# Performance work log

Measured on AMD Instinct MI355X. Metric: run time of the kernel, lower is better.

Reference implementation:

```python
import jax, jax.numpy as jnp
import numpy as np
import math

D_MODEL = 1024
N_HEADS = 16
HEAD_DIM = D_MODEL // N_HEADS
RANK = 128
SCALE = 1.0 / math.sqrt(HEAD_DIM)


def lowrank(x, u, v, b):
    # y = (x @ u) @ v + b : d_model -> rank -> d_model
    return jnp.einsum('bsd,dr,re->bse', x, u, v) + b


def setup_inputs() -> dict:
    key = jax.random.key(0)
    ks = jax.random.split(key, 16)
    B, S = 2, 2048
    inp = {
        'q': jax.random.normal(ks[0], (B, S, D_MODEL), jnp.float32),
        'k': jax.random.normal(ks[1], (B, S, D_MODEL), jnp.float32),
        'v': jax.random.normal(ks[2], (B, S, D_MODEL), jnp.float32),
        'mask': jnp.ones((B, S), jnp.int32),
    }
    i = 3
    for name in ('q', 'k', 'v', 'out'):
        inp[f'{name}_u'] = jax.random.normal(ks[i], (D_MODEL, RANK), jnp.float32) * 0.02
        inp[f'{name}_v'] = jax.random.normal(ks[i + 1], (RANK, D_MODEL), jnp.float32) * 0.02
        inp[f'{name}_b'] = jnp.zeros((D_MODEL,), jnp.float32)
        i += 2
    return inp


def reference(q, k, v, mask, q_u, q_v, q_b, k_u, k_v, k_b, v_u, v_v, v_b, out_u, out_v, out_b):
    B, S, _ = q.shape
    qh = lowrank(q, q_u, q_v, q_b).reshape(B, S, N_HEADS, HEAD_DIM)
    kh = lowrank(k, k_u, k_v, k_b).reshape(B, S, N_HEADS, HEAD_DIM)
    vh = lowrank(v, v_u, v_v, v_b).reshape(B, S, N_HEADS, HEAD_DIM)
    # scores: [B, H, Sq, Sk]
    scores = jnp.einsum('bqhd,bkhd->bhqk', qh, kh) * SCALE
    scores = jnp.where(mask[:, None, None, :] == 0, -1e9, scores)
    attn = jax.nn.softmax(scores, axis=-1)
    ctx = jnp.einsum('bhqk,bkhd->bqhd', attn, vh).reshape(B, S, D_MODEL)
    return lowrank(ctx, out_u, out_v, out_b)
```

## Files before the change

### kernel.cpp

```cpp
#include <hip/hip_runtime.h>
#include <hip/hip_bf16.h>
#include <stdint.h>

#define DEVI __device__ __forceinline__

typedef __attribute__((ext_vector_type(8))) __bf16 bf16x8;
typedef __attribute__((ext_vector_type(4))) float f32x4;
typedef __attribute__((ext_vector_type(4))) unsigned short us4;

DEVI unsigned short f2bf(float x) {
  union { __bf16 b; unsigned short s; } u;
  u.b = (__bf16)x;
  return u.s;
}

DEVI f32x4 mfma16(bf16x8 a, bf16x8 b, f32x4 c) {
  return __builtin_amdgcn_mfma_f32_16x16x32_bf16(a, b, c, 0, 0, 0);
}

DEVI f32x4 vmax4(f32x4 a, f32x4 b) {
  f32x4 r;
  r[0] = fmaxf(a[0], b[0]); r[1] = fmaxf(a[1], b[1]);
  r[2] = fmaxf(a[2], b[2]); r[3] = fmaxf(a[3], b[3]);
  return r;
}

DEVI bf16x8 ld_frag(const unsigned short* tile, int row, int ld, int kbase, int lane) {
  const unsigned short* p = tile + row * ld + kbase + ((lane >> 4) << 2);
  union { bf16x8 f; us4 h[2]; } u;
  u.h[0] = *(const us4*)p;
  u.h[1] = *(const us4*)(p + 16);
  return u.f;
}

struct TP { const float* in[8]; unsigned short* out[8]; };

__global__ __launch_bounds__(256) void wtrans2(TP p) {
  const int z = blockIdx.y;
  const int R = (z & 1) ? 128 : 1024;
  const int C = (z & 1) ? 1024 : 128;
  __shared__ unsigned short T[32][33];
  const int tilesC = C >> 5;
  const int tr0 = (blockIdx.x / tilesC) << 5;
  const int tc0 = (blockIdx.x % tilesC) << 5;
  const int tx = threadIdx.x & 31, ty = threadIdx.x >> 5;
  #pragma unroll
  for (int j = 0; j < 4; j++)
    T[ty + j * 8][tx] = f2bf(p.in[z][(size_t)(tr0 + ty + j * 8) * C + tc0 + tx]);
  __syncthreads();
  #pragma unroll
  for (int j = 0; j < 4; j++)
    p.out[z][(size_t)(tc0 + ty + j * 8) * R + tr0 + tx] = T[tx][ty + j * 8];
}

struct PJ {
  const void* X[3];
  const unsigned short* UT[3];
  const unsigned short* VT[3];
  const float* bias[3];
  void* O[3];
  float oscale[3];
};

template<bool ABF16, bool OF32>
__global__ __launch_bounds__(256)
void proj_fused(PJ p) {
  __shared__ unsigned short SH[128 * 132 + 64 * 132];
  unsigned short* Xs = SH;
  unsigned short* Us = SH + 64 * 36;
  unsigned short* Vs = SH;
  unsigned short* Ts = SH + 128 * 132;

  const int tid = threadIdx.x, lane = tid & 63, w = tid >> 6;
  const int z = blockIdx.z;
  const int m0 = blockIdx.x * 64;
  const int lg4 = (lane >> 4) << 2, l15 = lane & 15;

  const float* Xf = (const float*)p.X[z];
  const unsigned short* Xb = (const unsigned short*)p.X[z];
  const unsigned short* UT = p.UT[z];
  const unsigned short* VT = p.VT[z];

  const int xr = tid >> 2, xc = (tid & 3) * 8;
  const int ur = tid >> 1, uc = (tid & 1) * 16;

  float4 rx0, rx1; uint4 rxb;
  uint4 ru0, ru1;
  auto ldX = [&](int k0) {
    if (ABF16) {
      rxb = *(const uint4*)(Xb + (size_t)(m0 + xr) * 1024 + k0 + xc);
    } else {
      const float* s = Xf + (size_t)(m0 + xr) * 1024 + k0 + xc;
      rx0 = *(const float4*)s; rx1 = *(const float4*)(s + 4);
    }
    const unsigned short* su = UT + (size_t)ur * 1024 + k0 + uc;
    ru0 = *(const uint4*)su; ru1 = *(const uint4*)(su + 8);
  };

  f32x4 acc1[4][2] = {};
  ldX(0);
  for (int k0 = 0; k0 < 1024; k0 += 32) {
    __syncthreads();
    {
      union { uint4 u; us4 h[2]; } t;
      us4* xd = (us4*)&Xs[xr * 36 + xc];
      if (ABF16) {
        t.u = rxb; xd[0] = t.h[0]; xd[1] = t.h[1];
      } else {
        us4 a, bq;
        a[0] = f2bf(rx0.x); a[1] = f2bf(rx0.y); a[2] = f2bf(rx0.z); a[3] = f2bf(rx0.w);
        bq[0] = f2bf(rx1.x); bq[1] = f2bf(rx1.y); bq[2] = f2bf(rx1.z); bq[3] = f2bf(rx1.w);
        xd[0] = a; xd[1] = bq;
      }
      us4* udst = (us4*)&Us[ur * 36 + uc];
      t.u = ru0; udst[0] = t.h[0]; udst[1] = t.h[1];
      t.u = ru1; udst[2] = t.h[0]; udst[3] = t.h[1];
    }
    int kn = k0 + 32; if (kn > 992) kn = 992;
    ldX(kn);
    __syncthreads();

    bf16x8 af[4], wf[2];
    #pragma unroll
    for (int mi = 0; mi < 4; mi++)
      af[mi] = ld_frag(Xs, mi * 16 + l15, 36, 0, lane);
    #pragma unroll
    for (int ni = 0; ni < 2; ni++)
      wf[ni] = ld_frag(Us, w * 32 + ni * 16 + l15, 36, 0, lane);
    #pragma unroll
    for (int mi = 0; mi < 4; mi++)
      #pragma unroll
      for (int ni = 0; ni < 2; ni++)
        acc1[mi][ni] = mfma16(af[mi], wf[ni], acc1[mi][ni]);
  }

  #pragma unroll
  for (int mi = 0; mi < 4; mi++)
    #pragma unroll
    for (int ni = 0; ni < 2; ni++)
      #pragma unroll
      for (int r = 0; r < 4; r++)
        Ts[(mi * 16 + lg4 + r) * 132 + w * 32 + ni * 16 + l15] = f2bf(acc1[mi][ni][r]);
  __syncthreads();

  bf16x8 af2[4][4];
  #pragma unroll
  for (int mi = 0; mi < 4; mi++)
    #pragma unroll
    for (int kc = 0; kc < 4; kc++)
      af2[mi][kc] = ld_frag(Ts, mi * 16 + l15, 132, kc * 32, lane);

  const float os = p.oscale[z];
  const int vr = tid >> 2, vc = (tid & 3) * 32;
  for (int nc = 0; nc < 8; nc++) {
    __syncthreads();
    #pragma unroll
    for (int pp = 0; pp < 2; pp++) {
      const unsigned short* s = VT + (size_t)(nc * 128 + pp * 64 + vr) * 128 + vc;
      uint4* d = (uint4*)&Vs[(pp * 64 + vr) * 132 + vc];
      #pragma unroll
      for (int j = 0; j < 4; j++) d[j] = *(const uint4*)(s + j * 8);
    }
    __syncthreads();

    f32x4 acc2[4][2] = {};
    #pragma unroll
    for (int kc = 0; kc < 4; kc++) {
      bf16x8 bf0 = ld_frag(Vs, w * 32 + 0 * 16 + l15, 132, kc * 32, lane);
      bf16x8 bf1 = ld_frag(Vs, w * 32 + 1 * 16 + l15, 132, kc * 32, lane);
      #pragma unroll
      for (int mi = 0; mi < 4; mi++) {
        acc2[mi][0] = mfma16(af2[mi][kc], bf0, acc2[mi][0]);
        acc2[mi][1] = mfma16(af2[mi][kc], bf1, acc2[mi][1]);
      }
    }

    #pragma unroll
    for (int ni = 0; ni < 2; ni++) {
      const int col = nc * 128 + w * 32 + ni * 16 + l15;
      const float bv = p.bias[z][col];
      #pragma unroll
      for (int mi = 0; mi < 4; mi++)
        #pragma unroll
        for (int r = 0; r < 4; r++) {
          const int row = m0 + mi * 16 + lg4 + r;
          float vv = (acc2[mi][ni][r] + bv) * os;
          if (OF32) ((float*)p.O[z])[(size_t)row * 1024 + col] = vv;
          else ((unsigned short*)p.O[z])[(size_t)row * 1024 + col] = f2bf(vv);
        }
    }
  }
}

__global__ __launch_bounds__(512, 4)
void attn_k3(const unsigned short* __restrict__ qh, const unsigned short* __restrict__ kh,
             const unsigned short* __restrict__ vh, const int* __restrict__ mask,
             unsigned short* __restrict__ ctx) {
  const int S = 2048, DM = 1024;
  __shared__ unsigned short Ks[64][68];
  __shared__ unsigned short VTs[64][68];
  __shared__ alignas(16) float mkadd[64];
  const int tid = threadIdx.x, lane = tid & 63, w = tid >> 6;
  const int b = blockIdx.z, h = blockIdx.y, q0 = blockIdx.x * 128;
  const int lg4 = (lane >> 4) << 2, l15 = lane & 15;
  const int qrow = q0 + w * 16 + l15;

  bf16x8 qf[2];
  #pragma unroll
  for (int kk = 0; kk < 2; kk++) {
    const unsigned short* p = qh + (size_t)(b * S + qrow) * DM + h * 64 + kk * 32 + lg4;
    union { bf16x8 f; us4 h4[2]; } u;
    u.h4[0] = *(const us4*)p;
    u.h4[1] = *(const us4*)(p + 16);
    qf[kk] = u.f;
  }

  float mrow = -1e30f, lrow = 0.f;
  f32x4 acc_o[4] = {};

  const int srow = tid >> 3, sseg = (tid & 7) * 8;

  uint4 rk, rv; int rmI = 1;
  auto ldT = [&](int kv0) {
    rk = *(const uint4*)(kh + (size_t)(b * S + kv0 + srow) * DM + h * 64 + sseg);
    rv = *(const uint4*)(vh + (size_t)(b * S + kv0 + srow) * DM + h * 64 + sseg);
    if (tid < 64) rmI = mask[b * S + kv0 + tid];
  };
  ldT(0);

  for (int kv0 = 0; kv0 < S; kv0 += 64) {
    __syncthreads();
    {
      union { uint4 u; us4 h[2]; unsigned short s[8]; } tk, tv;
      tk.u = rk;
      us4* kd = (us4*)&Ks[srow][sseg];
      kd[0] = tk.h[0]; kd[1] = tk.h[1];
      tv.u = rv;
      #pragma unroll
      for (int j = 0; j < 8; j++) VTs[sseg + j][srow] = tv.s[j];
      if (tid < 64) mkadd[tid] = (rmI == 0) ? -1e9f : 0.0f;
    }
    int nxt = kv0 + 64; if (nxt >= S) nxt = kv0;
    ldT(nxt);
    __syncthreads();

    f32x4 sc[4];
    __builtin_amdgcn_s_setprio(1);
    #pragma unroll
    for (int mi = 0; mi < 4; mi++) {
      bf16x8 kf0 = ld_frag(&Ks[0][0], mi * 16 + l15, 68, 0, lane);
      bf16x8 kf1 = ld_frag(&Ks[0][0], mi * 16 + l15, 68, 32, lane);
      f32x4 zz = {0.f, 0.f, 0.f, 0.f};
      zz = mfma16(kf0, qf[0], zz);
      zz = mfma16(kf1, qf[1], zz);
      sc[mi] = zz;
    }
    __builtin_amdgcn_s_setprio(0);
    #pragma unroll
    for (int mi = 0; mi < 4; mi++)
      sc[mi] += *(const f32x4*)&mkadd[mi * 16 + lg4];

    f32x4 tm = vmax4(vmax4(sc[0], sc[1]), vmax4(sc[2], sc[3]));
    float pm = fmaxf(fmaxf(tm[0], tm[1]), fmaxf(tm[2], tm[3]));
    pm = fmaxf(pm, __shfl_xor(pm, 16));
    pm = fmaxf(pm, __shfl_xor(pm, 32));

    if (!__all(pm <= mrow + 8.f)) {
      const float mnew = fmaxf(mrow, pm);
      const float alpha = __expf(mrow - mnew);
      lrow *= alpha;
      #pragma unroll
      for (int mi = 0; mi < 4; mi++) acc_o[mi] *= alpha;
      mrow = mnew;
    }

    #pragma unroll
    for (int mi = 0; mi < 4; mi++)
      #pragma unroll
      for (int r = 0; r < 4; r++)
        sc[mi][r] = __expf(sc[mi][r] - mrow);

    f32x4 ssum = (sc[0] + sc[1]) + (sc[2] + sc[3]);
    float rs = (ssum[0] + ssum[1]) + (ssum[2] + ssum[3]);
    rs += __shfl_xor(rs, 16);
    rs += __shfl_xor(rs, 32);
    lrow += rs;

    bf16x8 pb[2];
    #pragma unroll
    for (int kc = 0; kc < 2; kc++) {
      bf16x8 f;
      #pragma unroll
      for (int e = 0; e < 8; e++)
        f[e] = (__bf16)sc[2 * kc + (e >> 2)][e & 3];
      pb[kc] = f;
    }

    __builtin_amdgcn_s_setprio(1);
    #pragma unroll
    for (int kc = 0; kc < 2; kc++)
      #pragma unroll
      for (int mi = 0; mi < 4; mi++) {
        bf16x8 va = ld_frag(&VTs[0][0], mi * 16 + l15, 68, kc * 32, lane);
        acc_o[mi] = mfma16(va, pb[kc], acc_o[mi]);
      }
    __builtin_amdgcn_s_setprio(0);
  }

  const float rinv = 1.0f / lrow;
  const size_t rowoff = (size_t)(b * S + qrow) * DM + h * 64;
  #pragma unroll
  for (int mi = 0; mi < 4; mi++) {
    us4 o;
    #pragma unroll
    for (int r = 0; r < 4; r++) o[r] = f2bf(acc_o[mi][r] * rinv);
    *(us4*)(ctx + rowoff + mi * 16 + lg4) = o;
  }
}

extern "C" void kernel_launch(void* const* d_in, const int* in_sizes, int n_in,
                              void* d_out, int out_size, void* d_ws, size_t ws_size,
                              hipStream_t stream) {
  const float* q = (const float*)d_in[0];
  const float* k = (const float*)d_in[1];
  const float* v = (const float*)d_in[2];
  const int* mask = (const int*)d_in[3];
  const float* wu[4] = {(const float*)d_in[4], (const float*)d_in[7],
                        (const float*)d_in[10], (const float*)d_in[13]};
  const float* wv[4] = {(const float*)d_in[5], (const float*)d_in[8],
                        (const float*)d_in[11], (const float*)d_in[14]};
  const float* wb[4] = {(const float*)d_in[6], (const float*)d_in[9],
                        (const float*)d_in[12], (const float*)d_in[15]};

  char* ws = (char*)d_ws;
  unsigned short* WT  = (unsigned short*)ws;
  unsigned short* QH  = (unsigned short*)(ws + 2097152);
  unsigned short* KH  = QH + 4194304;
  unsigned short* VH  = KH + 4194304;
  unsigned short* CTX = VH + 4194304;

  TP tp;
  for (int i = 0; i < 4; i++) { tp.in[2 * i] = wu[i]; tp.in[2 * i + 1] = wv[i]; }
  for (int i = 0; i < 8; i++) tp.out[i] = WT + (size_t)i * 131072;
  wtrans2<<<dim3(128, 8), 256, 0, stream>>>(tp);

  const float SCALE = 0.125f;

  PJ pq = {};
  pq.X[0] = q; pq.X[1] = k; pq.X[2] = v;
  pq.UT[0] = tp.out[0]; pq.UT[1] = tp.out[2]; pq.UT[2] = tp.out[4];
  pq.VT[0] = tp.out[1]; pq.VT[1] = tp.out[3]; pq.VT[2] = tp.out[5];
  pq.bias[0] = wb[0]; pq.bias[1] = wb[1]; pq.bias[2] = wb[2];
  pq.O[0] = QH; pq.O[1] = KH; pq.O[2] = VH;
  pq.oscale[0] = SCALE; pq.oscale[1] = 1.f; pq.oscale[2] = 1.f;
  proj_fused<false, false><<<dim3(64, 1, 3), 256, 0, stream>>>(pq);

  attn_k3<<<dim3(16, 16, 2), 512, 0, stream>>>(QH, KH, VH, mask, CTX);

  PJ po = {};
  po.X[0] = CTX;
  po.UT[0] = tp.out[6];
  po.VT[0] = tp.out[7];
  po.bias[0] = wb[3];
  po.O[0] = d_out;
  po.oscale[0] = 1.f;
  proj_fused<true, true><<<dim3(64, 1, 1), 256, 0, stream>>>(po);
}
```

Measured before the change: 256.8 us.

## Switch attention to 32x32x16 MFMA tiles with exp2 softmax and 256-row blocks

Rewrites the attention kernel to use 32x32x16 bf16 MFMA instead of 16x16x32, so each wave covers 32 query rows and each block 256 rows, halving the grid. The log2(e) factor is folded into the Q projection scale so the softmax can use exp2f. Exponentials are now computed against the old running max before the rescale check, with a correction multiply when the max grows. The aim is to cut LDS fragment loads and shuffle reductions per MFMA. In exchange there are more accumulator registers per wave and fewer blocks to spread across CUs.

```diff
diff --git a/kernel.cpp b/kernel.cpp
--- a/kernel.cpp
+++ b/kernel.cpp
@@ -6,6 +6,7 @@
 
 typedef __attribute__((ext_vector_type(8))) __bf16 bf16x8;
 typedef __attribute__((ext_vector_type(4))) float f32x4;
+typedef __attribute__((ext_vector_type(16))) float f32x16;
 typedef __attribute__((ext_vector_type(4))) unsigned short us4;
 
 DEVI unsigned short f2bf(float x) {
@@ -17,12 +18,8 @@
 DEVI f32x4 mfma16(bf16x8 a, bf16x8 b, f32x4 c) {
   return __builtin_amdgcn_mfma_f32_16x16x32_bf16(a, b, c, 0, 0, 0);
 }
-
-DEVI f32x4 vmax4(f32x4 a, f32x4 b) {
-  f32x4 r;
-  r[0] = fmaxf(a[0], b[0]); r[1] = fmaxf(a[1], b[1]);
-  r[2] = fmaxf(a[2], b[2]); r[3] = fmaxf(a[3], b[3]);
-  return r;
+DEVI f32x16 mfma32(bf16x8 a, bf16x8 b, f32x16 c) {
+  return __builtin_amdgcn_mfma_f32_32x32x16_bf16(a, b, c, 0, 0, 0);
 }
 
 DEVI bf16x8 ld_frag(const unsigned short* tile, int row, int ld, int kbase, int lane) {
@@ -30,6 +27,14 @@
   union { bf16x8 f; us4 h[2]; } u;
   u.h[0] = *(const us4*)p;
   u.h[1] = *(const us4*)(p + 16);
+  return u.f;
+}
+
+DEVI bf16x8 ld_frag32(const unsigned short* tile, int row, int ld, int kbase, int lane) {
+  const unsigned short* p = tile + row * ld + kbase + ((lane >> 5) << 2);
+  union { bf16x8 f; us4 h[2]; } u;
+  u.h[0] = *(const us4*)p;
+  u.h[1] = *(const us4*)(p + 8);
   return u.f;
 }
 
@@ -192,31 +197,31 @@
   }
 }
 
-__global__ __launch_bounds__(512, 4)
-void attn_k3(const unsigned short* __restrict__ qh, const unsigned short* __restrict__ kh,
+__global__ __launch_bounds__(512)
+void attn_k4(const unsigned short* __restrict__ qh, const unsigned short* __restrict__ kh,
              const unsigned short* __restrict__ vh, const int* __restrict__ mask,
              unsigned short* __restrict__ ctx) {
   const int S = 2048, DM = 1024;
-  __shared__ unsigned short Ks[64][68];
-  __shared__ unsigned short VTs[64][68];
+  __shared__ unsigned short Ks[64][70];
+  __shared__ unsigned short VTs[64][70];
   __shared__ alignas(16) float mkadd[64];
   const int tid = threadIdx.x, lane = tid & 63, w = tid >> 6;
-  const int b = blockIdx.z, h = blockIdx.y, q0 = blockIdx.x * 128;
-  const int lg4 = (lane >> 4) << 2, l15 = lane & 15;
-  const int qrow = q0 + w * 16 + l15;
-
-  bf16x8 qf[2];
-  #pragma unroll
-  for (int kk = 0; kk < 2; kk++) {
-    const unsigned short* p = qh + (size_t)(b * S + qrow) * DM + h * 64 + kk * 32 + lg4;
+  const int b = blockIdx.z, h = blockIdx.y, q0 = blockIdx.x * 256;
+  const int l31 = lane & 31, hi = lane >> 5;
+  const int qrow = q0 + w * 32 + l31;
+
+  bf16x8 qf[4];
+  #pragma unroll
+  for (int ks = 0; ks < 4; ks++) {
+    const unsigned short* p = qh + (size_t)(b * S + qrow) * DM + h * 64 + ks * 16 + hi * 4;
     union { bf16x8 f; us4 h4[2]; } u;
     u.h4[0] = *(const us4*)p;
-    u.h4[1] = *(const us4*)(p + 16);
-    qf[kk] = u.f;
+    u.h4[1] = *(const us4*)(p + 8);
+    qf[ks] = u.f;
   }
 
-  float mrow = -1e30f, lrow = 0.f;
-  f32x4 acc_o[4] = {};
+  float mrow = 0.f, lrow = 0.f;
+  f32x16 acc[2] = {};
 
   const int srow = tid >> 3, sseg = (tid & 7) * 8;
 
@@ -244,65 +249,77 @@
     ldT(nxt);
     __syncthreads();
 
-    f32x4 sc[4];
+    f32x16 sc[2];
     __builtin_amdgcn_s_setprio(1);
     #pragma unroll
-    for (int mi = 0; mi < 4; mi++) {
-      bf16x8 kf0 = ld_frag(&Ks[0][0], mi * 16 + l15, 68, 0, lane);
-      bf16x8 kf1 = ld_frag(&Ks[0][0], mi * 16 + l15, 68, 32, lane);
-      f32x4 zz = {0.f, 0.f, 0.f, 0.f};
-      zz = mfma16(kf0, qf[0], zz);
-      zz = mfma16(kf1, qf[1], zz);
-      sc[mi] = zz;
+    for (int mi = 0; mi < 2; mi++) {
+      f32x16 z = {};
+      #pragma unroll
+      for (int ks = 0; ks < 4; ks++) {
+        bf16x8 kf = ld_frag32(&Ks[0][0], mi * 32 + l31, 70, ks * 16, lane);
+        z = mfma32(kf, qf[ks], z);
+      }
+      sc[mi] = z;
     }
     __builtin_amdgcn_s_setprio(0);
-    #pragma unroll
-    for (int mi = 0; mi < 4; mi++)
-      sc[mi] += *(const f32x4*)&mkadd[mi * 16 + lg4];
-
-    f32x4 tm = vmax4(vmax4(sc[0], sc[1]), vmax4(sc[2], sc[3]));
-    float pm = fmaxf(fmaxf(tm[0], tm[1]), fmaxf(tm[2], tm[3]));
-    pm = fmaxf(pm, __shfl_xor(pm, 16));
+
+    #pragma unroll
+    for (int mi = 0; mi < 2; mi++)
+      #pragma unroll
+      for (int rr = 0; rr < 4; rr++) {
+        f32x4 mv = *(const f32x4*)&mkadd[mi * 32 + rr * 8 + hi * 4];
+        #pragma unroll
+        for (int j = 0; j < 4; j++) sc[mi][rr * 4 + j] += mv[j];
+      }
+
+    float pm = sc[0][0];
+    #pragma unroll
+    for (int r = 1; r < 16; r++) pm = fmaxf(pm, sc[0][r]);
+    #pragma unroll
+    for (int r = 0; r < 16; r++) pm = fmaxf(pm, sc[1][r]);
+
+    #pragma unroll
+    for (int mi = 0; mi < 2; mi++)
+      #pragma unroll
+      for (int r = 0; r < 16; r++)
+        sc[mi][r] = exp2f(sc[mi][r] - mrow);
+
     pm = fmaxf(pm, __shfl_xor(pm, 32));
 
     if (!__all(pm <= mrow + 8.f)) {
       const float mnew = fmaxf(mrow, pm);
-      const float alpha = __expf(mrow - mnew);
+      const float alpha = exp2f(mrow - mnew);
       lrow *= alpha;
       #pragma unroll
-      for (int mi = 0; mi < 4; mi++) acc_o[mi] *= alpha;
+      for (int mi = 0; mi < 2; mi++)
+        #pragma unroll
+        for (int r = 0; r < 16; r++) { acc[mi][r] *= alpha; sc[mi][r] *= alpha; }
       mrow = mnew;
     }
 
-    #pragma unroll
-    for (int mi = 0; mi < 4; mi++)
-      #pragma unroll
-      for (int r = 0; r < 4; r++)
-        sc[mi][r] = __expf(sc[mi][r] - mrow);
-
-    f32x4 ssum = (sc[0] + sc[1]) + (sc[2] + sc[3]);
-    float rs = (ssum[0] + ssum[1]) + (ssum[2] + ssum[3]);
-    rs += __shfl_xor(rs, 16);
+    float rs = 0.f;
+    #pragma unroll
+    for (int r = 0; r < 16; r++) rs += sc[0][r] + sc[1][r];
     rs += __shfl_xor(rs, 32);
     lrow += rs;
 
-    bf16x8 pb[2];
-    #pragma unroll
-    for (int kc = 0; kc < 2; kc++) {
+    bf16x8 pb[4];
+    #pragma unroll
+    for (int kc = 0; kc < 4; kc++) {
       bf16x8 f;
       #pragma unroll
       for (int e = 0; e < 8; e++)
-        f[e] = (__bf16)sc[2 * kc + (e >> 2)][e & 3];
+        f[e] = (__bf16)sc[kc >> 1][(kc & 1) * 8 + e];
       pb[kc] = f;
     }
 
     __builtin_amdgcn_s_setprio(1);
     #pragma unroll
-    for (int kc = 0; kc < 2; kc++)
-      #pragma unroll
-      for (int mi = 0; mi < 4; mi++) {
-        bf16x8 va = ld_frag(&VTs[0][0], mi * 16 + l15, 68, kc * 32, lane);
-        acc_o[mi] = mfma16(va, pb[kc], acc_o[mi]);
+    for (int mi = 0; mi < 2; mi++)
+      #pragma unroll
+      for (int kc = 0; kc < 4; kc++) {
+        bf16x8 va = ld_frag32(&VTs[0][0], mi * 32 + l31, 70, kc * 16, lane);
+        acc[mi] = mfma32(va, pb[kc], acc[mi]);
       }
     __builtin_amdgcn_s_setprio(0);
   }
@@ -310,12 +327,14 @@
   const float rinv = 1.0f / lrow;
   const size_t rowoff = (size_t)(b * S + qrow) * DM + h * 64;
   #pragma unroll
-  for (int mi = 0; mi < 4; mi++) {
-    us4 o;
-    #pragma unroll
-    for (int r = 0; r < 4; r++) o[r] = f2bf(acc_o[mi][r] * rinv);
-    *(us4*)(ctx + rowoff + mi * 16 + lg4) = o;
-  }
+  for (int mi = 0; mi < 2; mi++)
+    #pragma unroll
+    for (int rr = 0; rr < 4; rr++) {
+      us4 o;
+      #pragma unroll
+      for (int j = 0; j < 4; j++) o[j] = f2bf(acc[mi][rr * 4 + j] * rinv);
+      *(us4*)(ctx + rowoff + mi * 32 + rr * 8 + hi * 4) = o;
+    }
 }
 
 extern "C" void kernel_launch(void* const* d_in, const int* in_sizes, int n_in,
@@ -344,7 +363,7 @@
   for (int i = 0; i < 8; i++) tp.out[i] = WT + (size_t)i * 131072;
   wtrans2<<<dim3(128, 8), 256, 0, stream>>>(tp);
 
-  const float SCALE = 0.125f;
+  const float SCALE = 0.125f * 1.44269504f;
 
   PJ pq = {};
   pq.X[0] = q; pq.X[1] = k; pq.X[2] = v;
@@ -355,7 +374,7 @@
   pq.oscale[0] = SCALE; pq.oscale[1] = 1.f; pq.oscale[2] = 1.f;
   proj_fused<false, false><<<dim3(64, 1, 3), 256, 0, stream>>>(pq);
 
-  attn_k3<<<dim3(16, 16, 2), 512, 0, stream>>>(QH, KH, VH, mask, CTX);
+  attn_k4<<<dim3(8, 16, 2), 512, 0, stream>>>(QH, KH, VH, mask, CTX);
 
   PJ po = {};
   po.X[0] = CTX;
```

Result: slower. 458.9 us (+78.7%).

## Double-buffer K/V tiles in attention, use exp2 softmax, shrink blocks to 256 threads

Applied to the files above, without the earlier changes.

The attention kernel now keeps two shared-memory K/V buffers, so the next tile is written while the current one is consumed, cutting the per-tile barrier pairs to one. Blocks shrink from 512 to 256 threads with 64 query rows each, doubling the grid. log2(e) is folded into the Q scale so softmax can use exp2f, and the exponentials are computed before the cross-lane max reduction, then rescaled when the max grows. LDS row padding changes from 68 to 70 elements, and the running max starts at 0 rather than -inf. Together these aim to overlap loads with compute and shorten the softmax critical path, at the cost of more shared memory per block and extra rescale work when the max changes.

```diff
diff --git a/kernel.cpp b/kernel.cpp
--- a/kernel.cpp
+++ b/kernel.cpp
@@ -192,16 +192,16 @@
   }
 }
 
-__global__ __launch_bounds__(512, 4)
-void attn_k3(const unsigned short* __restrict__ qh, const unsigned short* __restrict__ kh,
+__global__ __launch_bounds__(256)
+void attn_k5(const unsigned short* __restrict__ qh, const unsigned short* __restrict__ kh,
              const unsigned short* __restrict__ vh, const int* __restrict__ mask,
              unsigned short* __restrict__ ctx) {
   const int S = 2048, DM = 1024;
-  __shared__ unsigned short Ks[64][68];
-  __shared__ unsigned short VTs[64][68];
-  __shared__ alignas(16) float mkadd[64];
+  __shared__ unsigned short Ks[2][64][70];
+  __shared__ unsigned short VTs[2][64][70];
+  __shared__ alignas(16) float mkadd[2][64];
   const int tid = threadIdx.x, lane = tid & 63, w = tid >> 6;
-  const int b = blockIdx.z, h = blockIdx.y, q0 = blockIdx.x * 128;
+  const int b = blockIdx.z, h = blockIdx.y, q0 = blockIdx.x * 64;
   const int lg4 = (lane >> 4) << 2, l15 = lane & 15;
   const int qrow = q0 + w * 16 + l15;
 
@@ -215,41 +215,49 @@
     qf[kk] = u.f;
   }
 
-  float mrow = -1e30f, lrow = 0.f;
+  float mrow = 0.f, lrow = 0.f;
   f32x4 acc_o[4] = {};
 
-  const int srow = tid >> 3, sseg = (tid & 7) * 8;
-
-  uint4 rk, rv; int rmI = 1;
+  const int srow = tid >> 2, sseg = (tid & 3) * 16;
+
+  uint4 rk0, rk1, rv0, rv1; int rmI = 1;
   auto ldT = [&](int kv0) {
-    rk = *(const uint4*)(kh + (size_t)(b * S + kv0 + srow) * DM + h * 64 + sseg);
-    rv = *(const uint4*)(vh + (size_t)(b * S + kv0 + srow) * DM + h * 64 + sseg);
+    const unsigned short* ks = kh + (size_t)(b * S + kv0 + srow) * DM + h * 64 + sseg;
+    rk0 = *(const uint4*)ks; rk1 = *(const uint4*)(ks + 8);
+    const unsigned short* vs = vh + (size_t)(b * S + kv0 + srow) * DM + h * 64 + sseg;
+    rv0 = *(const uint4*)vs; rv1 = *(const uint4*)(vs + 8);
     if (tid < 64) rmI = mask[b * S + kv0 + tid];
   };
+  auto wrT = [&](int buf) {
+    union { uint4 u[2]; us4 h[4]; unsigned short s[16]; } tk, tv;
+    tk.u[0] = rk0; tk.u[1] = rk1;
+    us4* kd = (us4*)&Ks[buf][srow][sseg];
+    kd[0] = tk.h[0]; kd[1] = tk.h[1]; kd[2] = tk.h[2]; kd[3] = tk.h[3];
+    tv.u[0] = rv0; tv.u[1] = rv1;
+    #pragma unroll
+    for (int j = 0; j < 16; j++) VTs[buf][sseg + j][srow] = tv.s[j];
+    if (tid < 64) mkadd[buf][tid] = (rmI == 0) ? -1e9f : 0.0f;
+  };
+
   ldT(0);
-
-  for (int kv0 = 0; kv0 < S; kv0 += 64) {
-    __syncthreads();
-    {
-      union { uint4 u; us4 h[2]; unsigned short s[8]; } tk, tv;
-      tk.u = rk;
-      us4* kd = (us4*)&Ks[srow][sseg];
-      kd[0] = tk.h[0]; kd[1] = tk.h[1];
-      tv.u = rv;
-      #pragma unroll
-      for (int j = 0; j < 8; j++) VTs[sseg + j][srow] = tv.s[j];
-      if (tid < 64) mkadd[tid] = (rmI == 0) ? -1e9f : 0.0f;
-    }
-    int nxt = kv0 + 64; if (nxt >= S) nxt = kv0;
-    ldT(nxt);
-    __syncthreads();
+  wrT(0);
+  ldT(64);
+
+  for (int t = 0; t < 32; t++) {
+    const int cur = t & 1;
+    __syncthreads();
+    if (t < 31) {
+      wrT(cur ^ 1);
+      int nx = t + 2; if (nx > 31) nx = 31;
+      ldT(nx * 64);
+    }
 
     f32x4 sc[4];
     __builtin_amdgcn_s_setprio(1);
     #pragma unroll
     for (int mi = 0; mi < 4; mi++) {
-      bf16x8 kf0 = ld_frag(&Ks[0][0], mi * 16 + l15, 68, 0, lane);
-      bf16x8 kf1 = ld_frag(&Ks[0][0], mi * 16 + l15, 68, 32, lane);
+      bf16x8 kf0 = ld_frag(&Ks[cur][0][0], mi * 16 + l15, 70, 0, lane);
+      bf16x8 kf1 = ld_frag(&Ks[cur][0][0], mi * 16 + l15, 70, 32, lane);
       f32x4 zz = {0.f, 0.f, 0.f, 0.f};
       zz = mfma16(kf0, qf[0], zz);
       zz = mfma16(kf1, qf[1], zz);
@@ -258,27 +266,32 @@
     __builtin_amdgcn_s_setprio(0);
     #pragma unroll
     for (int mi = 0; mi < 4; mi++)
-      sc[mi] += *(const f32x4*)&mkadd[mi * 16 + lg4];
+      sc[mi] += *(const f32x4*)&mkadd[cur][mi * 16 + lg4];
 
     f32x4 tm = vmax4(vmax4(sc[0], sc[1]), vmax4(sc[2], sc[3]));
     float pm = fmaxf(fmaxf(tm[0], tm[1]), fmaxf(tm[2], tm[3]));
+
+    #pragma unroll
+    for (int mi = 0; mi < 4; mi++)
+      #pragma unroll
+      for (int r = 0; r < 4; r++)
+        sc[mi][r] = exp2f(sc[mi][r] - mrow);
+
     pm = fmaxf(pm, __shfl_xor(pm, 16));
     pm = fmaxf(pm, __shfl_xor(pm, 32));
 
     if (!__all(pm <= mrow + 8.f)) {
       const float mnew = fmaxf(mrow, pm);
-      const float alpha = __expf(mrow - mnew);
+      const float alpha = exp2f(mrow - mnew);
       lrow *= alpha;
       #pragma unroll
-      for (int mi = 0; mi < 4; mi++) acc_o[mi] *= alpha;
+      for (int mi = 0; mi < 4; mi++) {
+        acc_o[mi] *= alpha;
+        #pragma unroll
+        for (int r = 0; r < 4; r++) sc[mi][r] *= alpha;
+      }
       mrow = mnew;
     }
-
-    #pragma unroll
-    for (int mi = 0; mi < 4; mi++)
-      #pragma unroll
-      for (int r = 0; r < 4; r++)
-        sc[mi][r] = __expf(sc[mi][r] - mrow);
 
     f32x4 ssum = (sc[0] + sc[1]) + (sc[2] + sc[3]);
     float rs = (ssum[0] + ssum[1]) + (ssum[2] + ssum[3]);
@@ -300,9 +313,9 @@
     #pragma unroll
     for (int kc = 0; kc < 2; kc++)
       #pragma unroll
-      for (int mi = 0; mi < 4; mi++) {
-        bf16x8 va = ld_frag(&VTs[0][0], mi * 16 + l15, 68, kc * 32, lane);
-        acc_o[mi] = mfma16(va, pb[kc], acc_o[mi]);
+      for (int di = 0; di < 4; di++) {
+        bf16x8 va = ld_frag(&VTs[cur][0][0], di * 16 + l15, 70, kc * 32, lane);
+        acc_o[di] = mfma16(va, pb[kc], acc_o[di]);
       }
     __builtin_amdgcn_s_setprio(0);
   }
@@ -310,11 +323,11 @@
   const float rinv = 1.0f / lrow;
   const size_t rowoff = (size_t)(b * S + qrow) * DM + h * 64;
   #pragma unroll
-  for (int mi = 0; mi < 4; mi++) {
+  for (int di = 0; di < 4; di++) {
     us4 o;
     #pragma unroll
-    for (int r = 0; r < 4; r++) o[r] = f2bf(acc_o[mi][r] * rinv);
-    *(us4*)(ctx + rowoff + mi * 16 + lg4) = o;
+    for (int r = 0; r < 4; r++) o[r] = f2bf(acc_o[di][r] * rinv);
+    *(us4*)(ctx + rowoff + di * 16 + lg4) = o;
   }
 }
 
@@ -344,7 +357,7 @@
   for (int i = 0; i < 8; i++) tp.out[i] = WT + (size_t)i * 131072;
   wtrans2<<<dim3(128, 8), 256, 0, stream>>>(tp);
 
-  const float SCALE = 0.125f;
+  const float SCALE = 0.125f * 1.44269504f;
 
   PJ pq = {};
   pq.X[0] = q; pq.X[1] = k; pq.X[2] = v;
@@ -355,7 +368,7 @@
   pq.oscale[0] = SCALE; pq.oscale[1] = 1.f; pq.oscale[2] = 1.f;
   proj_fused<false, false><<<dim3(64, 1, 3), 256, 0, stream>>>(pq);
 
-  attn_k3<<<dim3(16, 16, 2), 512, 0, stream>>>(QH, KH, VH, mask, CTX);
+  attn_k5<<<dim3(32, 16, 2), 256, 0, stream>>>(QH, KH, VH, mask, CTX);
 
   PJ po = {};
   po.X[0] = CTX;
```

After: 717.5 us. 2.79x slower.
